# Performance work log

Hardware: AMD Instinct MI355X
Metric: run time of the kernel (lower is better)

The kernel has to match this reference:

```python
import jax, jax.numpy as jnp
import numpy as np

DIM = 256; HEADS = 8; DK = 64; DV = 64; FH = 32; FW = 32; B = 16
INK = HEADS * DK; INV = HEADS * DV; N = FH * FW
SCALE = DK ** -0.5; EPS = 1e-5


def _pos_indices():
    pos = np.stack(np.meshgrid(np.arange(FH), np.arange(FW), indexing='ij'), axis=-1).reshape(-1, 2)
    rel = np.abs(pos[:, None, :] - pos[None, :, :])  # [N,N,2]
    return jnp.asarray(rel[..., 0] * FW + rel[..., 1], jnp.int32)  # [N,N]


def _bn(x, g, b, m, v):
    # eval-mode BatchNorm2d over channel axis 1
    s = (g / jnp.sqrt(v + EPS))
    return x * s[None, :, None, None] + (b - m * s)[None, :, None, None]


def setup_inputs() -> dict:
    key = jax.random.key(0)
    ks = jax.random.split(key, 24)
    f32 = jnp.float32
    def bn_params(k, c):
        k1, k2, k3, k4 = jax.random.split(k, 4)
        return (jax.random.normal(k1, (c,), f32) * 0.1 + 1.0,
                jax.random.normal(k2, (c,), f32) * 0.1,
                jax.random.normal(k3, (c,), f32) * 0.1,
                jax.random.uniform(k4, (c,), f32) + 0.5)
    gq, bq, mq, vq = bn_params(ks[1], INK)
    gk, bk, mk, vk = bn_params(ks[3], INK)
    gv, bv, mv, vv = bn_params(ks[5], INV)
    go, bo, mo, vo = bn_params(ks[7], DIM)
    return {
        'x': jax.random.normal(ks[0], (B, DIM, FH, FW), f32),
        'wq': jax.random.normal(ks[2], (INK, DIM), f32) * (DIM ** -0.5),
        'gq': gq, 'bq': bq, 'mq': mq, 'vq': vq,
        'wk': jax.random.normal(ks[4], (INK, DIM), f32) * (DIM ** -0.5),
        'gk': gk, 'bk': bk, 'mk': mk, 'vk': vk,
        'wv': jax.random.normal(ks[6], (INV, DIM), f32) * (DIM ** -0.5),
        'gv': gv, 'bv': bv, 'mv': mv, 'vv': vv,
        'emb': jax.random.normal(ks[8], (N, HEADS), f32) * 0.02,
        'w_out': jax.random.normal(ks[9], (DIM, INV), f32) * (INV ** -0.5),
        'b_out': jax.random.normal(ks[10], (DIM,), f32) * 0.02,
        'go': go, 'bo': bo, 'mo': mo, 'vo': vo,
        'pos_indices': _pos_indices(),
    }


def reference(x, wq, gq, bq, mq, vq, wk, gk, bk, mk, vk, wv, gv, bv, mv, vv,
              emb, w_out, b_out, go, bo, mo, vo, pos_indices):
    b = x.shape[0]
    # 1x1 conv == channel matmul
    q = _bn(jnp.einsum('bchw,oc->bohw', x, wq), gq, bq, mq, vq)
    k = _bn(jnp.einsum('bchw,oc->bohw', x, wk), gk, bk, mk, vk)
    v = _bn(jnp.einsum('bchw,oc->bohw', x, wv), gv, bv, mv, vv)
    # 'b (h d) x y -> b h (x y) d'
    def split_heads(t, d):
        return t.reshape(b, HEADS, d, N).transpose(0, 1, 3, 2)
    q = split_heads(q, DK); k = split_heads(k, DK); v = split_heads(v, DV)
    dots = jnp.einsum('bhid,bhjd->bhij', q, k) * SCALE  # [b,h,N,N]
    bias = emb[pos_indices]                               # [N,N,h] gather
    dots = dots + jnp.transpose(bias, (2, 0, 1))[None] / SCALE
    attn = jax.nn.softmax(dots, axis=-1)
    out = jnp.einsum('bhij,bhjd->bhid', attn, v)
    out = out.transpose(0, 1, 3, 2).reshape(b, INV, FH, FW)  # 'b h (x y) d -> b (h d) x y'
    hs = out * jnp.clip(out + 3.0, 0.0, 6.0) / 6.0           # Hardswish
    y = jnp.einsum('bchw,oc->bohw', hs, w_out) + b_out[None, :, None, None]
    return _bn(y, go, bo, mo, vo)
```

## Files before the change

### kernel.cpp

```cpp
#include <hip/hip_runtime.h>

typedef __attribute__((ext_vector_type(4))) float f32x4;
typedef __attribute__((ext_vector_type(8))) _Float16 f16x8;
typedef __attribute__((ext_vector_type(4))) _Float16 f16x4;

static __device__ __forceinline__ f32x4 mfma16f(f16x8 a, f16x8 b, f32x4 c) {
    return __builtin_amdgcn_mfma_f32_16x16x32_f16(a, b, c, 0, 0, 0);
}

__global__ __launch_bounds__(256) void prep(
    const float* __restrict__ x,
    const float* __restrict__ s0, const float* __restrict__ s1,
    const float* __restrict__ s2, const float* __restrict__ s3,
    _Float16* __restrict__ d0h, _Float16* __restrict__ d0l,
    _Float16* __restrict__ d1h, _Float16* __restrict__ d1l,
    _Float16* __restrict__ d2h, _Float16* __restrict__ d2l,
    _Float16* __restrict__ d3h, _Float16* __restrict__ d3l,
    _Float16* __restrict__ xth, _Float16* __restrict__ xtl)
{
    __shared__ float lt[32][36];
    const int t = threadIdx.x;
    const int bid = blockIdx.x;
    if (bid < 2048) {
        const int seg = bid >> 9;
        const int i = (bid & 511) * 256 + t;
        const float* src = (seg == 0) ? s0 : (seg == 1) ? s1 : (seg == 2) ? s2 : s3;
        _Float16* dh = (seg == 0) ? d0h : (seg == 1) ? d1h : (seg == 2) ? d2h : d3h;
        _Float16* dl = (seg == 0) ? d0l : (seg == 1) ? d1l : (seg == 2) ? d2l : d3l;
        const float f = src[i];
        const _Float16 h = (_Float16)f;
        dh[i] = h;
        dl[i] = (_Float16)(f - (float)h);
    } else {
        const int bid2 = bid - 2048;
        const int c0 = (bid2 & 7) * 32, hw0 = ((bid2 >> 3) & 31) * 32, b = bid2 >> 8;
        {
            const int cl = t >> 3, hw4 = (t & 7) * 4;
            *(f32x4*)&lt[cl][hw4] = *(const f32x4*)&x[((size_t)(b * 256 + c0 + cl)) * 1024 + hw0 + hw4];
        }
        __syncthreads();
        {
            const int hwl = t >> 3, c4 = (t & 7) * 4;
            f16x4 hv, lv;
#pragma unroll
            for (int e = 0; e < 4; ++e) {
                const float f = lt[c4 + e][hwl];
                const _Float16 h = (_Float16)f;
                hv[e] = h;
                lv[e] = (_Float16)(f - (float)h);
            }
            const size_t off = ((size_t)(b * 1024 + hw0 + hwl)) * 256 + c0 + c4;
            *(f16x4*)(xth + off) = hv;
            *(f16x4*)(xtl + off) = lv;
        }
    }
}

__global__ __launch_bounds__(256) void qkv_mfma(
    const _Float16* __restrict__ xth, const _Float16* __restrict__ xtl,
    const _Float16* __restrict__ wqh, const _Float16* __restrict__ wql,
    const _Float16* __restrict__ wkh, const _Float16* __restrict__ wkl,
    const _Float16* __restrict__ wvh, const _Float16* __restrict__ wvl,
    const float* __restrict__ gq, const float* __restrict__ bq, const float* __restrict__ mq, const float* __restrict__ vq,
    const float* __restrict__ gk, const float* __restrict__ bk, const float* __restrict__ mk, const float* __restrict__ vk,
    const float* __restrict__ gv, const float* __restrict__ bv, const float* __restrict__ mv, const float* __restrict__ vv,
    _Float16* __restrict__ qh, _Float16* __restrict__ ql,
    _Float16* __restrict__ kh,
    _Float16* __restrict__ vt)
{
    __shared__ _Float16 Ah[128][72];
    __shared__ _Float16 Al[128][72];
    __shared__ float sc_l[128], tc_l[128];

    const int t = threadIdx.x;
    const int bn = blockIdx.x;
    const int m0 = blockIdx.y * 128;
    const int proj = bn >> 2;
    const int o0 = (bn & 3) * 128;
    const int bimg = m0 >> 10;
    const int nb = m0 & 1023;

    const _Float16* Wh = (proj == 0) ? wqh : (proj == 1) ? wkh : wvh;
    const _Float16* Wl = (proj == 0) ? wql : (proj == 1) ? wkl : wvl;
    const float* G  = (proj == 0) ? gq : (proj == 1) ? gk : gv;
    const float* Bt = (proj == 0) ? bq : (proj == 1) ? bk : bv;
    const float* Mn = (proj == 0) ? mq : (proj == 1) ? mk : mv;
    const float* Vr = (proj == 0) ? vq : (proj == 1) ? vk : vv;

    if (t < 128) {
        const int o = o0 + t;
        float s = G[o] / sqrtf(Vr[o] + 1e-5f);
        float tt = Bt[o] - Mn[o] * s;
        if (proj == 0) { s *= 0.125f; tt *= 0.125f; }
        sc_l[t] = s; tc_l[t] = tt;
    }

    const int wave = t >> 6, lane = t & 63;
    const int quad = lane >> 4, l16 = lane & 15;
    const int wm = (wave >> 1) * 64, wn = (wave & 1) * 64;

    f32x4 acc[4][4] = {};

    for (int c0 = 0; c0 < 256; c0 += 64) {
        __syncthreads();
        {
            int r = t >> 3;
            const int cs = (t & 7) * 8;
#pragma unroll
            for (int p = 0; p < 4; ++p, r += 32) {
                const size_t off = ((size_t)(bimg * 1024 + nb + r)) * 256 + c0 + cs;
                *(f16x8*)&Ah[r][cs] = *(const f16x8*)(xth + off);
                *(f16x8*)&Al[r][cs] = *(const f16x8*)(xtl + off);
            }
        }
        __syncthreads();
#pragma unroll
        for (int kk = 0; kk < 2; ++kk) {
            f16x8 ah[4], al[4], bh[4], bl[4];
#pragma unroll
            for (int mi = 0; mi < 4; ++mi) {
                ah[mi] = *(const f16x8*)&Ah[wm + mi * 16 + l16][kk * 32 + quad * 8];
                al[mi] = *(const f16x8*)&Al[wm + mi * 16 + l16][kk * 32 + quad * 8];
            }
#pragma unroll
            for (int nj = 0; nj < 4; ++nj) {
                const size_t off = ((size_t)(o0 + wn + nj * 16 + l16)) * 256 + c0 + kk * 32 + quad * 8;
                bh[nj] = *(const f16x8*)(Wh + off);
                if (proj < 2) bl[nj] = *(const f16x8*)(Wl + off);
            }
            if (proj < 2) {
#pragma unroll
                for (int nj = 0; nj < 4; ++nj)
#pragma unroll
                    for (int mi = 0; mi < 4; ++mi) {
                        acc[nj][mi] = mfma16f(bh[nj], ah[mi], acc[nj][mi]);
                        acc[nj][mi] = mfma16f(bh[nj], al[mi], acc[nj][mi]);
                        acc[nj][mi] = mfma16f(bl[nj], ah[mi], acc[nj][mi]);
                    }
            } else {
#pragma unroll
                for (int mi = 0; mi < 4; ++mi)
#pragma unroll
                    for (int nj = 0; nj < 4; ++nj) {
                        acc[mi][nj] = mfma16f(ah[mi], bh[nj], acc[mi][nj]);
                        acc[mi][nj] = mfma16f(al[mi], bh[nj], acc[mi][nj]);
                    }
            }
        }
    }

    if (proj < 2) {
        _Float16* Oh = (proj == 0) ? qh : kh;
#pragma unroll
        for (int nj = 0; nj < 4; ++nj) {
            const int olb = wn + nj * 16 + quad * 4;
            const int ob = o0 + olb;
            const int head = ob >> 6, d0 = ob & 63;
#pragma unroll
            for (int mi = 0; mi < 4; ++mi) {
                const int n = nb + wm + mi * 16 + l16;
                f16x4 hv, lv;
#pragma unroll
                for (int rr = 0; rr < 4; ++rr) {
                    const float val = acc[nj][mi][rr] * sc_l[olb + rr] + tc_l[olb + rr];
                    const _Float16 h = (_Float16)val;
                    hv[rr] = h;
                    lv[rr] = (_Float16)(val - (float)h);
                }
                const size_t off = (((size_t)(bimg * 8 + head)) * 1024 + n) * 64 + d0;
                *(f16x4*)(Oh + off) = hv;
                if (proj == 0) *(f16x4*)(ql + off) = lv;
            }
        }
    } else {
#pragma unroll
        for (int nj = 0; nj < 4; ++nj) {
            const int olb = wn + nj * 16 + l16;
            const int o = o0 + olb;
            const int head = o >> 6, d = o & 63;
            const float s = sc_l[olb], tt = tc_l[olb];
#pragma unroll
            for (int mi = 0; mi < 4; ++mi) {
                const int n0 = nb + wm + mi * 16 + quad * 4;
                f16x4 v4;
#pragma unroll
                for (int rr = 0; rr < 4; ++rr) v4[rr] = (_Float16)(acc[mi][nj][rr] * s + tt);
                *(f16x4*)(vt + (((size_t)(bimg * 8 + head)) * 64 + d) * 1024 + n0) = v4;
            }
        }
    }
}

__global__ __launch_bounds__(256, 3) void attn_mfma(
    const _Float16* __restrict__ qh, const _Float16* __restrict__ ql,
    const _Float16* __restrict__ kh,
    const _Float16* __restrict__ vt,
    const float* __restrict__ emb,
    _Float16* __restrict__ hsh)
{
    __shared__ float    emb_s[1024];
    __shared__ _Float16 kth[64][76];
    __shared__ _Float16 vts[64][76];

    const int t = threadIdx.x;
    const int bid = blockIdx.x;
    const int bh = bid & 127, qb = bid >> 7;
    const int b = bh >> 3, h = bh & 7;
    const int wave = t >> 6, lane = t & 63;
    const int quad = lane >> 4, l16 = lane & 15;
    const int q0 = qb * 128 + wave * 32;
    const float L2E = 1.44269504f;

    for (int i = t; i < 1024; i += 256) emb_s[i] = (8.0f * emb[i * 8 + h] - 12.0f) * L2E;

    const size_t base = (size_t)bh * 65536;

    f16x8 qfh[2][2], qfl[2][2];
#pragma unroll
    for (int mi = 0; mi < 2; ++mi)
#pragma unroll
        for (int kk = 0; kk < 2; ++kk) {
            const size_t off = base + (size_t)(q0 + mi * 16 + l16) * 64 + kk * 32 + quad * 8;
            qfh[mi][kk] = *(const f16x8*)(qh + off);
            qfl[mi][kk] = *(const f16x8*)(ql + off);
        }

    int xi[2], yi[2];
#pragma unroll
    for (int mi = 0; mi < 2; ++mi) {
        const int ig = q0 + mi * 16 + l16;
        xi[mi] = ig >> 5;
        yi[mi] = ig & 31;
    }

    const int sr = t >> 3;
    const int scs = (t & 7) * 8;
    const int rv = t >> 2;
    const int cv = (t & 3) * 16;

    f16x8 pkh[2], pvv[2];
#pragma unroll
    for (int p = 0; p < 2; ++p) {
        pkh[p] = *(const f16x8*)(kh + base + (size_t)(p * 32 + sr) * 64 + scs);
        pvv[p] = *(const f16x8*)(vt + base + (size_t)rv * 1024 + cv + p * 8);
    }

    f32x4 ao[2][4] = {};
    float lsum[2] = {};

    for (int jb = 0; jb < 16; ++jb) {
        __syncthreads();
#pragma unroll
        for (int p = 0; p < 2; ++p) {
            *(f16x8*)&kth[p * 32 + sr][scs] = pkh[p];
            *(f16x8*)&vts[rv][cv + p * 8] = pvv[p];
        }
        __syncthreads();
        if (jb < 15) {
#pragma unroll
            for (int p = 0; p < 2; ++p) {
                pkh[p] = *(const f16x8*)(kh + base + (size_t)((jb + 1) * 64 + p * 32 + sr) * 64 + scs);
                pvv[p] = *(const f16x8*)(vt + base + (size_t)rv * 1024 + (jb + 1) * 64 + cv + p * 8);
            }
        }

#pragma unroll
        for (int nj = 0; nj < 4; ++nj) {
            const f16x8 kf0 = *(const f16x8*)&kth[nj * 16 + l16][quad * 8];
            const f16x8 kf1 = *(const f16x8*)&kth[nj * 16 + l16][32 + quad * 8];

            f32x4 ss[2] = {};
#pragma unroll
            for (int mi = 0; mi < 2; ++mi) {
                ss[mi] = mfma16f(kf0, qfh[mi][0], ss[mi]);
                ss[mi] = mfma16f(kf0, qfl[mi][0], ss[mi]);
                ss[mi] = mfma16f(kf1, qfh[mi][1], ss[mi]);
                ss[mi] = mfma16f(kf1, qfl[mi][1], ss[mi]);
            }

            const int xj = 2 * jb + (nj >> 1);
            const int yj0 = ((nj & 1) << 4) + quad * 4;
            f16x4 pa[2];
#pragma unroll
            for (int mi = 0; mi < 2; ++mi) {
                const int dxo = abs(xi[mi] - xj) << 5;
                const int yq = yi[mi] - yj0;
                const float p0 = exp2f(fmaf(ss[mi][0], L2E, emb_s[dxo + abs(yq)]));
                const float p1 = exp2f(fmaf(ss[mi][1], L2E, emb_s[dxo + abs(yq - 1)]));
                const float p2 = exp2f(fmaf(ss[mi][2], L2E, emb_s[dxo + abs(yq - 2)]));
                const float p3 = exp2f(fmaf(ss[mi][3], L2E, emb_s[dxo + abs(yq - 3)]));
                lsum[mi] += (p0 + p1) + (p2 + p3);
                f16x4 pv;
                pv[0] = (_Float16)p0; pv[1] = (_Float16)p1;
                pv[2] = (_Float16)p2; pv[3] = (_Float16)p3;
                pa[mi] = pv;
            }

            f16x4 vf[4];
#pragma unroll
            for (int dj = 0; dj < 4; ++dj)
                vf[dj] = *(const f16x4*)&vts[dj * 16 + l16][nj * 16 + quad * 4];
#pragma unroll
            for (int mi = 0; mi < 2; ++mi)
#pragma unroll
                for (int dj = 0; dj < 4; ++dj)
                    ao[mi][dj] = __builtin_amdgcn_mfma_f32_16x16x16f16(pa[mi], vf[dj], ao[mi][dj], 0, 0, 0);
        }
    }

#pragma unroll
    for (int mi = 0; mi < 2; ++mi) {
        float l = lsum[mi];
        l += __shfl_xor(l, 16, 64);
        l += __shfl_xor(l, 32, 64);
        float inv[4];
#pragma unroll
        for (int r = 0; r < 4; ++r)
            inv[r] = 1.0f / __shfl(l, quad * 4 + r, 64);
#pragma unroll
        for (int r = 0; r < 4; ++r) {
            const int ig = q0 + mi * 16 + quad * 4 + r;
#pragma unroll
            for (int dj = 0; dj < 4; ++dj) {
                const float o = ao[mi][dj][r] * inv[r];
                const float hsw = o * fminf(fmaxf(o + 3.0f, 0.0f), 6.0f) * (1.0f / 6.0f);
                hsh[((size_t)(b * 1024 + ig)) * 512 + h * 64 + dj * 16 + l16] = (_Float16)hsw;
            }
        }
    }
}

__global__ __launch_bounds__(256) void out_mfma(
    const _Float16* __restrict__ hsh,
    const _Float16* __restrict__ woh, const _Float16* __restrict__ wol,
    const float* __restrict__ b_out, const float* __restrict__ go, const float* __restrict__ bo,
    const float* __restrict__ mo, const float* __restrict__ vo, float* __restrict__ y)
{
    __shared__ _Float16 Ah[64][136];

    const int t = threadIdx.x;
    const int m0 = blockIdx.x * 64;
    const int o0 = blockIdx.y * 128;
    const int bimg = m0 >> 10, nb = m0 & 1023;
    const int wave = t >> 6, lane = t & 63;
    const int quad = lane >> 4, l16 = lane & 15;
    const int wm = (wave >> 1) * 32, wn = (wave & 1) * 64;

    f32x4 acc[2][4] = {};
    f16x8 bh[4], bl[4], nbh[4], nbl[4];

#pragma unroll
    for (int nj = 0; nj < 4; ++nj) {
        const size_t off = ((size_t)(o0 + wn + nj * 16 + l16)) * 512 + quad * 8;
        bh[nj] = *(const f16x8*)(woh + off);
        bl[nj] = *(const f16x8*)(wol + off);
    }

#pragma unroll
    for (int it = 0; it < 16; ++it) {
        const int c0 = (it >> 2) * 128, kk = it & 3;
        if (kk == 0) {
            __syncthreads();
            const int cs = (t & 7) * 16;
#pragma unroll
            for (int p = 0; p < 2; ++p) {
                const int r = (t >> 3) + p * 32;
                *(f16x8*)&Ah[r][cs]     = *(const f16x8*)(hsh + ((size_t)(m0 + r)) * 512 + c0 + cs);
                *(f16x8*)&Ah[r][cs + 8] = *(const f16x8*)(hsh + ((size_t)(m0 + r)) * 512 + c0 + cs + 8);
            }
            __syncthreads();
        }
        if (it < 15) {
            const int nit = it + 1;
            const int nc0 = (nit >> 2) * 128, nkk = nit & 3;
#pragma unroll
            for (int nj = 0; nj < 4; ++nj) {
                const size_t off = ((size_t)(o0 + wn + nj * 16 + l16)) * 512 + nc0 + nkk * 32 + quad * 8;
                nbh[nj] = *(const f16x8*)(woh + off);
                nbl[nj] = *(const f16x8*)(wol + off);
            }
        }
        f16x8 ah[2];
#pragma unroll
        for (int mi = 0; mi < 2; ++mi)
            ah[mi] = *(const f16x8*)&Ah[wm + mi * 16 + l16][kk * 32 + quad * 8];
#pragma unroll
        for (int mi = 0; mi < 2; ++mi)
#pragma unroll
            for (int nj = 0; nj < 4; ++nj) {
                acc[mi][nj] = mfma16f(ah[mi], bh[nj], acc[mi][nj]);
                acc[mi][nj] = mfma16f(ah[mi], bl[nj], acc[mi][nj]);
            }
#pragma unroll
        for (int nj = 0; nj < 4; ++nj) { bh[nj] = nbh[nj]; bl[nj] = nbl[nj]; }
    }

#pragma unroll
    for (int nj = 0; nj < 4; ++nj) {
        const int o = o0 + wn + nj * 16 + l16;
        const float s = go[o] / sqrtf(vo[o] + 1e-5f);
        const float tt = bo[o] - mo[o] * s;
        const float bf = b_out[o];
#pragma unroll
        for (int mi = 0; mi < 2; ++mi) {
            const int hw = nb + wm + mi * 16 + quad * 4;
            f32x4 v4;
#pragma unroll
            for (int rr = 0; rr < 4; ++rr) v4[rr] = (acc[mi][nj][rr] + bf) * s + tt;
            *(f32x4*)&y[((size_t)(bimg * 256 + o)) * 1024 + hw] = v4;
        }
    }
}

extern "C" void kernel_launch(void* const* d_in, const int* in_sizes, int n_in,
                              void* d_out, int out_size, void* d_ws, size_t ws_size,
                              hipStream_t stream) {
    const float* x     = (const float*)d_in[0];
    const float* wq    = (const float*)d_in[1];
    const float* gq    = (const float*)d_in[2];
    const float* bq    = (const float*)d_in[3];
    const float* mq    = (const float*)d_in[4];
    const float* vq    = (const float*)d_in[5];
    const float* wk    = (const float*)d_in[6];
    const float* gk    = (const float*)d_in[7];
    const float* bk    = (const float*)d_in[8];
    const float* mk    = (const float*)d_in[9];
    const float* vk    = (const float*)d_in[10];
    const float* wv    = (const float*)d_in[11];
    const float* gv    = (const float*)d_in[12];
    const float* bv    = (const float*)d_in[13];
    const float* mv    = (const float*)d_in[14];
    const float* vv    = (const float*)d_in[15];
    const float* emb   = (const float*)d_in[16];
    const float* w_out = (const float*)d_in[17];
    const float* b_out = (const float*)d_in[18];
    const float* go    = (const float*)d_in[19];
    const float* bo    = (const float*)d_in[20];
    const float* mo    = (const float*)d_in[21];
    const float* vo    = (const float*)d_in[22];

    _Float16* us = (_Float16*)d_ws;
    _Float16* xth = us;
    _Float16* xtl = us + 4194304;
    _Float16* hsh = us;
    _Float16* wsp = us + 16777216;
    _Float16* wqh = wsp,            *wql = wsp + 131072;
    _Float16* wkh = wsp + 262144,   *wkl = wsp + 393216;
    _Float16* wvh = wsp + 524288,   *wvl = wsp + 655360;
    _Float16* woh = wsp + 786432,   *wol = wsp + 917504;
    _Float16* qv  = us + 17825792;
    _Float16* qhw = qv,             *qlw = qv + 8388608;
    _Float16* khw = qv + 16777216;
    _Float16* vtw = qv + 33554432;

    prep<<<6144, 256, 0, stream>>>(x, wq, wk, wv, w_out,
                                   wqh, wql, wkh, wkl, wvh, wvl, woh, wol,
                                   xth, xtl);

    qkv_mfma<<<dim3(12, 128), 256, 0, stream>>>(
        xth, xtl, wqh, wql, wkh, wkl, wvh, wvl,
        gq, bq, mq, vq, gk, bk, mk, vk, gv, bv, mv, vv,
        qhw, qlw, khw, vtw);

    attn_mfma<<<1024, 256, 0, stream>>>(
        qhw, qlw, khw, vtw, emb, hsh);

    out_mfma<<<dim3(256, 2), 256, 0, stream>>>(
        hsh, woh, wol, b_out, go, bo, mo, vo, (float*)d_out);
}
```

Before: 299.5 us.

## Use 8 waves of 16 queries each in attention kernel, raise occupancy

```diff
diff --git a/kernel.cpp b/kernel.cpp
--- a/kernel.cpp
+++ b/kernel.cpp
@@ -191,7 +191,7 @@
     }
 }
 
-__global__ __launch_bounds__(256, 3) void attn_mfma(
+__global__ __launch_bounds__(512, 8) void attn_mfma(
     const _Float16* __restrict__ qh, const _Float16* __restrict__ ql,
     const _Float16* __restrict__ kh,
     const _Float16* __restrict__ vt,
@@ -208,60 +208,42 @@
     const int b = bh >> 3, h = bh & 7;
     const int wave = t >> 6, lane = t & 63;
     const int quad = lane >> 4, l16 = lane & 15;
-    const int q0 = qb * 128 + wave * 32;
+    const int q0 = qb * 128 + wave * 16;
     const float L2E = 1.44269504f;
 
-    for (int i = t; i < 1024; i += 256) emb_s[i] = (8.0f * emb[i * 8 + h] - 12.0f) * L2E;
+    for (int i = t; i < 1024; i += 512) emb_s[i] = (8.0f * emb[i * 8 + h] - 12.0f) * L2E;
 
     const size_t base = (size_t)bh * 65536;
 
-    f16x8 qfh[2][2], qfl[2][2];
-#pragma unroll
-    for (int mi = 0; mi < 2; ++mi)
-#pragma unroll
-        for (int kk = 0; kk < 2; ++kk) {
-            const size_t off = base + (size_t)(q0 + mi * 16 + l16) * 64 + kk * 32 + quad * 8;
-            qfh[mi][kk] = *(const f16x8*)(qh + off);
-            qfl[mi][kk] = *(const f16x8*)(ql + off);
-        }
-
-    int xi[2], yi[2];
-#pragma unroll
-    for (int mi = 0; mi < 2; ++mi) {
-        const int ig = q0 + mi * 16 + l16;
-        xi[mi] = ig >> 5;
-        yi[mi] = ig & 31;
-    }
+    f16x8 qfh[2], qfl[2];
+#pragma unroll
+    for (int kk = 0; kk < 2; ++kk) {
+        const size_t off = base + (size_t)(q0 + l16) * 64 + kk * 32 + quad * 8;
+        qfh[kk] = *(const f16x8*)(qh + off);
+        qfl[kk] = *(const f16x8*)(ql + off);
+    }
+
+    const int ig0 = q0 + l16;
+    const int xi = ig0 >> 5, yi = ig0 & 31;
 
     const int sr = t >> 3;
     const int scs = (t & 7) * 8;
-    const int rv = t >> 2;
-    const int cv = (t & 3) * 16;
-
-    f16x8 pkh[2], pvv[2];
-#pragma unroll
-    for (int p = 0; p < 2; ++p) {
-        pkh[p] = *(const f16x8*)(kh + base + (size_t)(p * 32 + sr) * 64 + scs);
-        pvv[p] = *(const f16x8*)(vt + base + (size_t)rv * 1024 + cv + p * 8);
-    }
-
-    f32x4 ao[2][4] = {};
-    float lsum[2] = {};
+
+    f16x8 pkh, pvv;
+    pkh = *(const f16x8*)(kh + base + (size_t)sr * 64 + scs);
+    pvv = *(const f16x8*)(vt + base + (size_t)sr * 1024 + scs);
+
+    f32x4 ao[4] = {};
+    float lsum = 0.0f;
 
     for (int jb = 0; jb < 16; ++jb) {
         __syncthreads();
-#pragma unroll
-        for (int p = 0; p < 2; ++p) {
-            *(f16x8*)&kth[p * 32 + sr][scs] = pkh[p];
-            *(f16x8*)&vts[rv][cv + p * 8] = pvv[p];
-        }
+        *(f16x8*)&kth[sr][scs] = pkh;
+        *(f16x8*)&vts[sr][scs] = pvv;
         __syncthreads();
         if (jb < 15) {
-#pragma unroll
-            for (int p = 0; p < 2; ++p) {
-                pkh[p] = *(const f16x8*)(kh + base + (size_t)((jb + 1) * 64 + p * 32 + sr) * 64 + scs);
-                pvv[p] = *(const f16x8*)(vt + base + (size_t)rv * 1024 + (jb + 1) * 64 + cv + p * 8);
-            }
+            pkh = *(const f16x8*)(kh + base + (size_t)((jb + 1) * 64 + sr) * 64 + scs);
+            pvv = *(const f16x8*)(vt + base + (size_t)sr * 1024 + (jb + 1) * 64 + scs);
         }
 
 #pragma unroll
@@ -269,63 +251,54 @@
             const f16x8 kf0 = *(const f16x8*)&kth[nj * 16 + l16][quad * 8];
             const f16x8 kf1 = *(const f16x8*)&kth[nj * 16 + l16][32 + quad * 8];
 
-            f32x4 ss[2] = {};
-#pragma unroll
-            for (int mi = 0; mi < 2; ++mi) {
-                ss[mi] = mfma16f(kf0, qfh[mi][0], ss[mi]);
-                ss[mi] = mfma16f(kf0, qfl[mi][0], ss[mi]);
-                ss[mi] = mfma16f(kf1, qfh[mi][1], ss[mi]);
-                ss[mi] = mfma16f(kf1, qfl[mi][1], ss[mi]);
-            }
+            f32x4 ss = {};
+            __builtin_amdgcn_s_setprio(1);
+            ss = mfma16f(kf0, qfh[0], ss);
+            ss = mfma16f(kf0, qfl[0], ss);
+            ss = mfma16f(kf1, qfh[1], ss);
+            ss = mfma16f(kf1, qfl[1], ss);
+            __builtin_amdgcn_s_setprio(0);
 
             const int xj = 2 * jb + (nj >> 1);
             const int yj0 = ((nj & 1) << 4) + quad * 4;
-            f16x4 pa[2];
-#pragma unroll
-            for (int mi = 0; mi < 2; ++mi) {
-                const int dxo = abs(xi[mi] - xj) << 5;
-                const int yq = yi[mi] - yj0;
-                const float p0 = exp2f(fmaf(ss[mi][0], L2E, emb_s[dxo + abs(yq)]));
-                const float p1 = exp2f(fmaf(ss[mi][1], L2E, emb_s[dxo + abs(yq - 1)]));
-                const float p2 = exp2f(fmaf(ss[mi][2], L2E, emb_s[dxo + abs(yq - 2)]));
-                const float p3 = exp2f(fmaf(ss[mi][3], L2E, emb_s[dxo + abs(yq - 3)]));
-                lsum[mi] += (p0 + p1) + (p2 + p3);
-                f16x4 pv;
-                pv[0] = (_Float16)p0; pv[1] = (_Float16)p1;
-                pv[2] = (_Float16)p2; pv[3] = (_Float16)p3;
-                pa[mi] = pv;
-            }
+            const int dxo = abs(xi - xj) << 5;
+            const int yq = yi - yj0;
+            const float p0 = __builtin_amdgcn_exp2f(fmaf(ss[0], L2E, emb_s[dxo + abs(yq)]));
+            const float p1 = __builtin_amdgcn_exp2f(fmaf(ss[1], L2E, emb_s[dxo + abs(yq - 1)]));
+            const float p2 = __builtin_amdgcn_exp2f(fmaf(ss[2], L2E, emb_s[dxo + abs(yq - 2)]));
+            const float p3 = __builtin_amdgcn_exp2f(fmaf(ss[3], L2E, emb_s[dxo + abs(yq - 3)]));
+            lsum += (p0 + p1) + (p2 + p3);
+            f16x4 pa;
+            pa[0] = (_Float16)p0; pa[1] = (_Float16)p1;
+            pa[2] = (_Float16)p2; pa[3] = (_Float16)p3;
 
             f16x4 vf[4];
 #pragma unroll
             for (int dj = 0; dj < 4; ++dj)
                 vf[dj] = *(const f16x4*)&vts[dj * 16 + l16][nj * 16 + quad * 4];
-#pragma unroll
-            for (int mi = 0; mi < 2; ++mi)
-#pragma unroll
-                for (int dj = 0; dj < 4; ++dj)
-                    ao[mi][dj] = __builtin_amdgcn_mfma_f32_16x16x16f16(pa[mi], vf[dj], ao[mi][dj], 0, 0, 0);
-        }
-    }
-
-#pragma unroll
-    for (int mi = 0; mi < 2; ++mi) {
-        float l = lsum[mi];
-        l += __shfl_xor(l, 16, 64);
-        l += __shfl_xor(l, 32, 64);
-        float inv[4];
-#pragma unroll
-        for (int r = 0; r < 4; ++r)
-            inv[r] = 1.0f / __shfl(l, quad * 4 + r, 64);
-#pragma unroll
-        for (int r = 0; r < 4; ++r) {
-            const int ig = q0 + mi * 16 + quad * 4 + r;
-#pragma unroll
-            for (int dj = 0; dj < 4; ++dj) {
-                const float o = ao[mi][dj][r] * inv[r];
-                const float hsw = o * fminf(fmaxf(o + 3.0f, 0.0f), 6.0f) * (1.0f / 6.0f);
-                hsh[((size_t)(b * 1024 + ig)) * 512 + h * 64 + dj * 16 + l16] = (_Float16)hsw;
-            }
+            __builtin_amdgcn_s_setprio(1);
+#pragma unroll
+            for (int dj = 0; dj < 4; ++dj)
+                ao[dj] = __builtin_amdgcn_mfma_f32_16x16x16f16(pa, vf[dj], ao[dj], 0, 0, 0);
+            __builtin_amdgcn_s_setprio(0);
+        }
+    }
+
+    float l = lsum;
+    l += __shfl_xor(l, 16, 64);
+    l += __shfl_xor(l, 32, 64);
+    float inv[4];
+#pragma unroll
+    for (int r = 0; r < 4; ++r)
+        inv[r] = 1.0f / __shfl(l, quad * 4 + r, 64);
+#pragma unroll
+    for (int r = 0; r < 4; ++r) {
+        const int ig = q0 + quad * 4 + r;
+#pragma unroll
+        for (int dj = 0; dj < 4; ++dj) {
+            const float o = ao[dj][r] * inv[r];
+            const float hsw = o * fminf(fmaxf(o + 3.0f, 0.0f), 6.0f) * (1.0f / 6.0f);
+            hsh[((size_t)(b * 1024 + ig)) * 512 + h * 64 + dj * 16 + l16] = (_Float16)hsw;
         }
     }
 }
@@ -462,7 +435,7 @@
         gq, bq, mq, vq, gk, bk, mk, vk, gv, bv, mv, vv,
         qhw, qlw, khw, vtw);
 
-    attn_mfma<<<1024, 256, 0, stream>>>(
+    attn_mfma<<<1024, 512, 0, stream>>>(
         qhw, qlw, khw, vtw, emb, hsh);
 
     out_mfma<<<dim3(256, 2), 256, 0, stream>>>(
```

Measured after the change: 450.7 us. +50.5%, slower.
